# Kernel tuning notes

Hardware: AMD Instinct MI355X
Metric: run time of the kernel (lower is better)

Reference implementation:

```python
import jax, jax.numpy as jnp
import numpy as np

N, CH, K, B = 30000, 96, 81, 8
HIDDEN = max(CH // 4, 8)
EPS = 1e-5


def setup_inputs() -> dict:
    key = jax.random.key(0)
    ks = jax.random.split(key, 12)
    feats = jax.random.normal(ks[0], (N, CH), dtype=jnp.float32)
    nbr_idx = jax.random.randint(ks[1], (N, K), 0, N).astype(jnp.int32)
    batch_ids = jnp.sort(jax.random.randint(ks[2], (N,), 0, B)).astype(jnp.int32)
    s = 1.0 / np.sqrt(CH * 1.0)
    W1 = jax.random.normal(ks[3], (K, CH, CH), dtype=jnp.float32) * s
    W2 = jax.random.normal(ks[4], (K, CH, CH), dtype=jnp.float32) * s
    g1 = jnp.ones((CH,), jnp.float32); b1 = jnp.zeros((CH,), jnp.float32)
    g2 = jnp.ones((CH,), jnp.float32); b2 = jnp.zeros((CH,), jnp.float32)
    fc1_w = jax.random.normal(ks[5], (CH, HIDDEN), dtype=jnp.float32) * s
    fc1_b = jnp.zeros((HIDDEN,), jnp.float32)
    fc2_w = jax.random.normal(ks[6], (HIDDEN, CH), dtype=jnp.float32) * (1.0 / np.sqrt(HIDDEN * 1.0))
    fc2_b = jnp.zeros((CH,), jnp.float32)
    return {"feats": feats, "W1": W1, "g1": g1, "b1": b1, "W2": W2,
            "g2": g2, "b2": b2, "fc1_w": fc1_w, "fc1_b": fc1_b,
            "fc2_w": fc2_w, "fc2_b": fc2_b, "nbr_idx": nbr_idx,
            "batch_ids": batch_ids}


def _sparse_conv(x, W, nbr):
    # gather-matmul-scatter form of MinkowskiConvolution (kernel map shared):
    # g: [N, K, ch] gathered neighbor features; contract each offset's [ch,ch] weight.
    g = x[nbr]
    return jnp.einsum('nkc,kcd->nd', g, W)


def _bn(x, gamma, beta):
    mu = jnp.mean(x, axis=0)
    var = jnp.var(x, axis=0)
    return gamma * (x - mu) * jax.lax.rsqrt(var + EPS) + beta


def _se(x, batch_ids, fc1_w, fc1_b, fc2_w, fc2_b):
    # MinkowskiGlobalAvgPooling: per-sample mean over points
    sums = jax.ops.segment_sum(x, batch_ids, num_segments=B)
    cnts = jax.ops.segment_sum(jnp.ones((x.shape[0], 1), x.dtype), batch_ids, num_segments=B)
    pooled = sums / jnp.maximum(cnts, 1.0)  # [B, ch]
    w = jax.nn.relu(pooled @ fc1_w + fc1_b)
    w = jax.nn.sigmoid(w @ fc2_w + fc2_b)   # [B, ch]
    return x * w[batch_ids]                  # broadcast multiplication


def reference(feats, W1, g1, b1, W2, g2, b2, fc1_w, fc1_b, fc2_w, fc2_b,
              nbr_idx, batch_ids):
    out = jax.nn.relu(_bn(_sparse_conv(feats, W1, nbr_idx), g1, b1))
    out = _bn(_sparse_conv(out, W2, nbr_idx), g2, b2)
    out = _se(out, batch_ids, fc1_w, fc1_b, fc2_w, fc2_b)
    return jax.nn.relu(out + feats)
```

## Files before the change

### kernel.cpp

```cpp
#include <hip/hip_runtime.h>
#include <hip/hip_bf16.h>

#define NPTS 30000
#define CH 96
#define KOFF 81
#define NB 8
#define HID 24
#define EPSV 1e-5f
#define NTILE 469
#define RT 3
#define RSPLIT 157
#define KSPLIT 4

typedef __attribute__((ext_vector_type(8))) short bf16x8;
typedef __attribute__((ext_vector_type(4))) float f32x4;

__device__ __forceinline__ ushort f2bf(float f) {
    union { float f; unsigned int u; } x; x.f = f;
    unsigned int u = x.u;
    unsigned int r = (u + 0x7fffu + ((u >> 16) & 1u)) >> 16;
    return (ushort)r;
}

__device__ __forceinline__ void gll16(const void* g, void* l) {
    __builtin_amdgcn_global_load_lds(
        (const __attribute__((address_space(1))) unsigned int*)g,
        (__attribute__((address_space(3))) unsigned int*)l, 16, 0, 0);
}

__global__ __launch_bounds__(256) void k_prep(const float* __restrict__ feats,
                                              const float* __restrict__ W1,
                                              const float* __restrict__ W2,
                                              const int* __restrict__ nbr,
                                              ushort* __restrict__ featsbf,
                                              float* __restrict__ outbuf,
                                              int* __restrict__ nbrT,
                                              ushort* __restrict__ wt1,
                                              ushort* __restrict__ wt2) {
    __shared__ __align__(16) char smem[36864];
    int bid = blockIdx.x, tid = threadIdx.x;
    if (bid < 2813) {
        int t = bid * 256 + tid;
        if (t < 720000) {
            float4 v = reinterpret_cast<const float4*>(feats)[t];
            ushort4 o;
            o.x = f2bf(v.x); o.y = f2bf(v.y); o.z = f2bf(v.z); o.w = f2bf(v.w);
            reinterpret_cast<ushort4*>(featsbf)[t] = o;
            float4 z = {0.f, 0.f, 0.f, 0.f};
            reinterpret_cast<float4*>(outbuf)[t] = z;
        }
    } else if (bid < 3282) {
        int* lds = (int*)smem;
        int n0 = (bid - 2813) * 64;
        int rows = min(64, NPTS - n0);
        int cnt = rows * 81;
        for (int i = tid; i < cnt; i += 256) lds[i] = nbr[n0 * 81 + i];
        __syncthreads();
        for (int o = tid; o < cnt; o += 256) {
            int kk = o / rows, r = o - kk * rows;
            nbrT[kk * NPTS + n0 + r] = lds[r * 81 + kk];
        }
    } else {
        float* lds = (float*)smem;
        int b = bid - 3282;
        int k = (b < 81) ? b : b - 81;
        const float* src = ((b < 81) ? W1 : W2) + k * 9216;
        ushort* dst = ((b < 81) ? wt1 : wt2) + k * 9216;
        for (int j = tid; j < 9216; j += 256) lds[j] = src[j];
        __syncthreads();
        for (int o = tid; o < 9216; o += 256) {
            int q = o / 768, rem = o - q * 768, d = rem >> 3, j = rem & 7;
            dst[o] = f2bf(lds[(q * 8 + j) * 96 + d]);
        }
    }
}

__global__ __launch_bounds__(256, 2) void k_conv(const ushort* __restrict__ xbf,
                                                 const ushort* __restrict__ wt,
                                                 const int* __restrict__ nbrT,
                                                 float* __restrict__ out) {
    __shared__ __align__(16) ushort Wsm[2][9216];

    const int tid = threadIdx.x;
    const int slice = blockIdx.x / RSPLIT;
    const int rb = blockIdx.x % RSPLIT;
    const int k0 = slice * 20;
    const int k1 = k0 + ((slice == 3) ? 21 : 20);
    const int wave = tid >> 6, lane = tid & 63;
    const int r16 = lane & 15, kg = lane >> 4;
    const int tile0 = rb * RT;

    int nrow[RT];
#pragma unroll
    for (int rt = 0; rt < RT; ++rt) {
        int n = (tile0 + rt) * 64 + wave * 16 + r16;
        nrow[rt] = (n < NPTS) ? n : (NPTS - 1);
    }

    f32x4 zero4 = {0.f, 0.f, 0.f, 0.f};
    f32x4 acc[RT][6];
#pragma unroll
    for (int rt = 0; rt < RT; ++rt)
#pragma unroll
        for (int db = 0; db < 6; ++db) acc[rt][db] = zero4;

    {
        const ushort* wsrc = wt + k0 * 9216 + lane * 8;
#pragma unroll
        for (int t = 0; t < 5; ++t) {
            int i = wave + t * 4;
            if (i < 18) gll16(wsrc + i * 512, Wsm[0] + i * 512);
        }
    }
    int idx[RT];
#pragma unroll
    for (int rt = 0; rt < RT; ++rt) idx[rt] = nbrT[k0 * NPTS + nrow[rt]];
    __syncthreads();

    int cur = 0;
    for (int k = k0; k < k1; ++k) {
        bf16x8 bfrag[18];
#pragma unroll
        for (int c = 0; c < 3; ++c) {
            int q = c * 4 + kg;
#pragma unroll
            for (int db = 0; db < 6; ++db)
                bfrag[c * 6 + db] = *reinterpret_cast<const bf16x8*>(
                    &Wsm[cur][q * 768 + (db * 16 + r16) * 8]);
        }
        bf16x8 afrag[RT][3];
#pragma unroll
        for (int rt = 0; rt < RT; ++rt) {
            const ushort* as = xbf + idx[rt] * 96 + kg * 8;
#pragma unroll
            for (int c = 0; c < 3; ++c)
                afrag[rt][c] = *reinterpret_cast<const bf16x8*>(as + c * 32);
        }
        if (k + 1 < k1) {
            const ushort* wsrc = wt + (k + 1) * 9216 + lane * 8;
#pragma unroll
            for (int t = 0; t < 5; ++t) {
                int i = wave + t * 4;
                if (i < 18) gll16(wsrc + i * 512, Wsm[cur ^ 1] + i * 512);
            }
#pragma unroll
            for (int rt = 0; rt < RT; ++rt) idx[rt] = nbrT[(k + 1) * NPTS + nrow[rt]];
        }
#pragma unroll
        for (int rt = 0; rt < RT; ++rt)
#pragma unroll
            for (int c = 0; c < 3; ++c)
#pragma unroll
                for (int db = 0; db < 6; ++db)
                    acc[rt][db] = __builtin_amdgcn_mfma_f32_16x16x32_bf16(
                        afrag[rt][c], bfrag[c * 6 + db], acc[rt][db], 0, 0, 0);
        __syncthreads();
        cur ^= 1;
    }

#pragma unroll
    for (int rt = 0; rt < RT; ++rt) {
        int rbase = (tile0 + rt) * 64 + wave * 16 + kg * 4;
#pragma unroll
        for (int db = 0; db < 6; ++db) {
            int col = db * 16 + r16;
#pragma unroll
            for (int i = 0; i < 4; ++i) {
                int r = rbase + i;
                if (r < NPTS) atomicAdd(&out[r * 96 + col], acc[rt][db][i]);
            }
        }
    }
}

__device__ __forceinline__ int lowb(const int* __restrict__ bids, int v) {
    int lo = 0, hi = NPTS;
    while (lo < hi) { int m = (lo + hi) >> 1; if (bids[m] < v) lo = m + 1; else hi = m; }
    return lo;
}

template <bool SEG>
__global__ __launch_bounds__(256) void k_stats(const float* __restrict__ y,
                                               const int* __restrict__ bids,
                                               float* __restrict__ ssum,
                                               float* __restrict__ ssq,
                                               float* __restrict__ segsum,
                                               float* __restrict__ cntf) {
    __shared__ float ls[96], lq[96], lg[96];
    int tid = threadIdx.x;
    if (tid < 96) { ls[tid] = 0.f; lq[tid] = 0.f; lg[tid] = 0.f; }
    __syncthreads();

    int b = 0, j, s, e;
    if (SEG) {
        b = blockIdx.x >> 5; j = blockIdx.x & 31;
        s = lowb(bids, b); e = lowb(bids, b + 1);
    } else {
        j = blockIdx.x; s = 0; e = NPTS;
    }
    const int stride = SEG ? (32 * 256) : (256 * 256);
    const int total = (e - s) * 24;
    const int base4 = s * 24;
    const int c40 = j * 256 + tid;

    f32x4 z = {0.f, 0.f, 0.f, 0.f};
    f32x4 sm[3] = {z, z, z}, sq[3] = {z, z, z};
    for (int c4 = c40; c4 < total; c4 += 3 * stride) {
#pragma unroll
        for (int m = 0; m < 3; ++m) {
            int c = c4 + m * stride;
            if (c < total) {
                f32x4 v = reinterpret_cast<const f32x4*>(y)[base4 + c];
                sm[m] += v; sq[m] += v * v;
            }
        }
    }
#pragma unroll
    for (int m = 0; m < 3; ++m) {
        int d0 = ((c40 + m * stride) * 4) % 96;
#pragma unroll
        for (int w = 0; w < 4; ++w) {
            atomicAdd(&ls[d0 + w], sm[m][w]);
            atomicAdd(&lq[d0 + w], sq[m][w]);
            if (SEG) atomicAdd(&lg[d0 + w], sm[m][w]);
        }
    }
    __syncthreads();
    if (tid < 96) {
        atomicAdd(&ssum[tid], ls[tid]);
        atomicAdd(&ssq[tid], lq[tid]);
        if (SEG) atomicAdd(&segsum[b * 96 + tid], lg[tid]);
    }
    if (SEG && tid == 0 && (blockIdx.x & 31) == 0) cntf[b] = (float)(e - s);
}

__global__ void k_bnfinal(const float* __restrict__ ssum, const float* __restrict__ ssq,
                          const float* __restrict__ g, const float* __restrict__ b,
                          float* __restrict__ scale, float* __restrict__ shift) {
    int t = threadIdx.x;
    if (t >= 96) return;
    float mean = ssum[t] * (1.0f / NPTS);
    float var = ssq[t] * (1.0f / NPTS) - mean * mean;
    float sc = g[t] * rsqrtf(var + EPSV);
    scale[t] = sc;
    shift[t] = b[t] - mean * sc;
}

__global__ void k_apply1(float* __restrict__ x, const float* __restrict__ scale,
                         const float* __restrict__ shift, ushort* __restrict__ h) {
    int t = blockIdx.x * 256 + threadIdx.x;
    if (t >= 720000) return;
    float4 v = reinterpret_cast<const float4*>(x)[t];
    int d0 = (t * 4) % 96;
    ushort4 o;
    o.x = f2bf(fmaxf(v.x * scale[d0] + shift[d0], 0.f));
    o.y = f2bf(fmaxf(v.y * scale[d0 + 1] + shift[d0 + 1], 0.f));
    o.z = f2bf(fmaxf(v.z * scale[d0 + 2] + shift[d0 + 2], 0.f));
    o.w = f2bf(fmaxf(v.w * scale[d0 + 3] + shift[d0 + 3], 0.f));
    reinterpret_cast<ushort4*>(h)[t] = o;
    float4 z = {0.f, 0.f, 0.f, 0.f};
    reinterpret_cast<float4*>(x)[t] = z;
}

__global__ void k_se(const float* __restrict__ segsum, const float* __restrict__ cnt,
                     const float* __restrict__ scale, const float* __restrict__ shift,
                     const float* __restrict__ fc1w, const float* __restrict__ fc1b,
                     const float* __restrict__ fc2w, const float* __restrict__ fc2b,
                     float* __restrict__ sew) {
    __shared__ float pooled[NB][96];
    __shared__ float hid[NB][HID];
    int t = threadIdx.x;
    for (int i = t; i < NB * 96; i += 256) {
        int b = i / 96, d = i - b * 96;
        pooled[b][d] = segsum[i] / fmaxf(cnt[b], 1.f) * scale[d] + shift[d];
    }
    __syncthreads();
    if (t < NB * HID) {
        int b = t / HID, h = t - b * HID;
        float s = fc1b[h];
        for (int d = 0; d < 96; ++d) s += pooled[b][d] * fc1w[d * HID + h];
        hid[b][h] = fmaxf(s, 0.f);
    }
    __syncthreads();
    for (int i = t; i < NB * 96; i += 256) {
        int b = i / 96, d = i - b * 96;
        float s = fc2b[d];
        for (int h = 0; h < HID; ++h) s += hid[b][h] * fc2w[h * 96 + d];
        sew[i] = 1.f / (1.f + expf(-s));
    }
}

__global__ void k_final(const float* __restrict__ out2, const float* __restrict__ feats,
                        const float* __restrict__ scale, const float* __restrict__ shift,
                        const float* __restrict__ sew, const int* __restrict__ bids,
                        float* __restrict__ out) {
    int t = blockIdx.x * 256 + threadIdx.x;
    if (t >= 720000) return;
    int e0 = t * 4;
    int n = e0 / 96;
    int d0 = e0 - n * 96;
    int b = bids[n];
    const float* w = sew + b * 96;
    float4 v = reinterpret_cast<const float4*>(out2)[t];
    float4 f = reinterpret_cast<const float4*>(feats)[t];
    float4 o;
    o.x = fmaxf((v.x * scale[d0] + shift[d0]) * w[d0] + f.x, 0.f);
    o.y = fmaxf((v.y * scale[d0 + 1] + shift[d0 + 1]) * w[d0 + 1] + f.y, 0.f);
    o.z = fmaxf((v.z * scale[d0 + 2] + shift[d0 + 2]) * w[d0 + 2] + f.z, 0.f);
    o.w = fmaxf((v.w * scale[d0 + 3] + shift[d0 + 3]) * w[d0 + 3] + f.w, 0.f);
    reinterpret_cast<float4*>(out)[t] = o;
}


extern "C" void kernel_launch(void* const* d_in, const int* in_sizes, int n_in,
                              void* d_out, int out_size, void* d_ws, size_t ws_size,
                              hipStream_t stream) {
    const float* feats = (const float*)d_in[0];
    const float* W1 = (const float*)d_in[1];
    const float* g1 = (const float*)d_in[2];
    const float* b1 = (const float*)d_in[3];
    const float* W2 = (const float*)d_in[4];
    const float* g2 = (const float*)d_in[5];
    const float* b2 = (const float*)d_in[6];
    const float* fc1w = (const float*)d_in[7];
    const float* fc1b = (const float*)d_in[8];
    const float* fc2w = (const float*)d_in[9];
    const float* fc2b = (const float*)d_in[10];
    const int* nbr = (const int*)d_in[11];
    const int* bids = (const int*)d_in[12];
    float* out = (float*)d_out;

    char* ws = (char*)d_ws;
    ushort* featsbf = (ushort*)(ws + 0);
    ushort* wt1 = (ushort*)(ws + 5760000);
    ushort* wt2 = (ushort*)(ws + 7252992);
    int* nbrT = (int*)(ws + 8745984);
    float* outbuf = (float*)(ws + 18465984);
    ushort* h1bf = (ushort*)(ws + 29985984);
    float* small = (float*)(ws + 35745984);
    float* sum1 = small + 0;
    float* sq1 = small + 96;
    float* sum2 = small + 192;
    float* sq2 = small + 288;
    float* scale1 = small + 384;
    float* shift1 = small + 480;
    float* scale2 = small + 576;
    float* shift2 = small + 672;
    float* segsum = small + 768;
    float* cntf = small + 1536;
    float* sew = small + 1544;

    const int gE = 2813;
    const int gC = KSPLIT * RSPLIT;

    hipMemsetAsync(small, 0, 16384, stream);
    k_prep<<<3444, 256, 0, stream>>>(feats, W1, W2, nbr, featsbf, outbuf, nbrT, wt1, wt2);

    k_conv<<<gC, 256, 0, stream>>>(featsbf, wt1, nbrT, outbuf);
    k_stats<false><<<256, 256, 0, stream>>>(outbuf, bids, sum1, sq1, segsum, cntf);
    k_bnfinal<<<1, 128, 0, stream>>>(sum1, sq1, g1, b1, scale1, shift1);
    k_apply1<<<gE, 256, 0, stream>>>(outbuf, scale1, shift1, h1bf);

    k_conv<<<gC, 256, 0, stream>>>(h1bf, wt2, nbrT, outbuf);
    k_stats<true><<<256, 256, 0, stream>>>(outbuf, bids, sum2, sq2, segsum, cntf);
    k_bnfinal<<<1, 128, 0, stream>>>(sum2, sq2, g2, b2, scale2, shift2);

    k_se<<<1, 256, 0, stream>>>(segsum, cntf, scale2, shift2, fc1w, fc1b, fc2w, fc2b, sew);
    k_final<<<gE, 256, 0, stream>>>(outbuf, feats, scale2, shift2, sew, bids, out);
}
```

Measured before the change: 370.8 us.

## Split conv over 8 kernel-offset slices and fold BN finalize into consumers

The conv grid doubles its split over kernel offsets (8 slices of about 10 offsets) and launch bounds now request 4 blocks per SM, to raise occupancy and parallelism. The gather loads of neighbour features are issued before the LDS weight-fragment reads, so global latency overlaps with the LDS reads. The separate single-block BN-finalize kernels are removed. Each block of k_apply1, k_se and k_final now recomputes scale and shift into shared memory, saving two launches at the cost of redundant per-block work and an extra barrier. Doubling the K-split doubles atomic or partial-sum traffic into the output buffer, and the higher occupancy target may force register spills given the large per-thread accumulator and fragment arrays.

Measured after the change: 1.266 ms. 241% more time.

```diff
diff --git a/kernel.cpp b/kernel.cpp
--- a/kernel.cpp
+++ b/kernel.cpp
@@ -10,7 +10,7 @@
 #define NTILE 469
 #define RT 3
 #define RSPLIT 157
-#define KSPLIT 4
+#define KSPLIT 8
 
 typedef __attribute__((ext_vector_type(8))) short bf16x8;
 typedef __attribute__((ext_vector_type(4))) float f32x4;
@@ -26,6 +26,22 @@
     __builtin_amdgcn_global_load_lds(
         (const __attribute__((address_space(1))) unsigned int*)g,
         (__attribute__((address_space(3))) unsigned int*)l, 16, 0, 0);
+}
+
+__device__ __forceinline__ void bn_coeffs(const float* __restrict__ ssum,
+                                          const float* __restrict__ ssq,
+                                          const float* __restrict__ g,
+                                          const float* __restrict__ b,
+                                          float* s_scale, float* s_shift) {
+    int t = threadIdx.x;
+    if (t < 96) {
+        float mean = ssum[t] * (1.0f / NPTS);
+        float var = ssq[t] * (1.0f / NPTS) - mean * mean;
+        float sc = g[t] * rsqrtf(var + EPSV);
+        s_scale[t] = sc;
+        s_shift[t] = b[t] - mean * sc;
+    }
+    __syncthreads();
 }
 
 __global__ __launch_bounds__(256) void k_prep(const float* __restrict__ feats,
@@ -75,7 +91,7 @@
     }
 }
 
-__global__ __launch_bounds__(256, 2) void k_conv(const ushort* __restrict__ xbf,
+__global__ __launch_bounds__(256, 4) void k_conv(const ushort* __restrict__ xbf,
                                                  const ushort* __restrict__ wt,
                                                  const int* __restrict__ nbrT,
                                                  float* __restrict__ out) {
@@ -84,8 +100,8 @@
     const int tid = threadIdx.x;
     const int slice = blockIdx.x / RSPLIT;
     const int rb = blockIdx.x % RSPLIT;
-    const int k0 = slice * 20;
-    const int k1 = k0 + ((slice == 3) ? 21 : 20);
+    const int k0 = slice * 10;
+    const int k1 = k0 + ((slice == 7) ? 11 : 10);
     const int wave = tid >> 6, lane = tid & 63;
     const int r16 = lane & 15, kg = lane >> 4;
     const int tile0 = rb * RT;
@@ -119,6 +135,14 @@
 
     int cur = 0;
     for (int k = k0; k < k1; ++k) {
+        bf16x8 afrag[RT][3];
+#pragma unroll
+        for (int rt = 0; rt < RT; ++rt) {
+            const ushort* as = xbf + idx[rt] * 96 + kg * 8;
+#pragma unroll
+            for (int c = 0; c < 3; ++c)
+                afrag[rt][c] = *reinterpret_cast<const bf16x8*>(as + c * 32);
+        }
         bf16x8 bfrag[18];
 #pragma unroll
         for (int c = 0; c < 3; ++c) {
@@ -127,14 +151,6 @@
             for (int db = 0; db < 6; ++db)
                 bfrag[c * 6 + db] = *reinterpret_cast<const bf16x8*>(
                     &Wsm[cur][q * 768 + (db * 16 + r16) * 8]);
-        }
-        bf16x8 afrag[RT][3];
-#pragma unroll
-        for (int rt = 0; rt < RT; ++rt) {
-            const ushort* as = xbf + idx[rt] * 96 + kg * 8;
-#pragma unroll
-            for (int c = 0; c < 3; ++c)
-                afrag[rt][c] = *reinterpret_cast<const bf16x8*>(as + c * 32);
         }
         if (k + 1 < k1) {
             const ushort* wsrc = wt + (k + 1) * 9216 + lane * 8;
@@ -234,20 +250,12 @@
     if (SEG && tid == 0 && (blockIdx.x & 31) == 0) cntf[b] = (float)(e - s);
 }
 
-__global__ void k_bnfinal(const float* __restrict__ ssum, const float* __restrict__ ssq,
-                          const float* __restrict__ g, const float* __restrict__ b,
-                          float* __restrict__ scale, float* __restrict__ shift) {
-    int t = threadIdx.x;
-    if (t >= 96) return;
-    float mean = ssum[t] * (1.0f / NPTS);
-    float var = ssq[t] * (1.0f / NPTS) - mean * mean;
-    float sc = g[t] * rsqrtf(var + EPSV);
-    scale[t] = sc;
-    shift[t] = b[t] - mean * sc;
-}
-
-__global__ void k_apply1(float* __restrict__ x, const float* __restrict__ scale,
-                         const float* __restrict__ shift, ushort* __restrict__ h) {
+__global__ void k_apply1(float* __restrict__ x,
+                         const float* __restrict__ ssum, const float* __restrict__ ssq,
+                         const float* __restrict__ g, const float* __restrict__ b,
+                         ushort* __restrict__ h) {
+    __shared__ float scale[96], shift[96];
+    bn_coeffs(ssum, ssq, g, b, scale, shift);
     int t = blockIdx.x * 256 + threadIdx.x;
     if (t >= 720000) return;
     float4 v = reinterpret_cast<const float4*>(x)[t];
@@ -263,44 +271,50 @@
 }
 
 __global__ void k_se(const float* __restrict__ segsum, const float* __restrict__ cnt,
-                     const float* __restrict__ scale, const float* __restrict__ shift,
+                     const float* __restrict__ ssum, const float* __restrict__ ssq,
+                     const float* __restrict__ g, const float* __restrict__ b,
                      const float* __restrict__ fc1w, const float* __restrict__ fc1b,
                      const float* __restrict__ fc2w, const float* __restrict__ fc2b,
                      float* __restrict__ sew) {
+    __shared__ float scale[96], shift[96];
     __shared__ float pooled[NB][96];
     __shared__ float hid[NB][HID];
+    bn_coeffs(ssum, ssq, g, b, scale, shift);
     int t = threadIdx.x;
     for (int i = t; i < NB * 96; i += 256) {
-        int b = i / 96, d = i - b * 96;
-        pooled[b][d] = segsum[i] / fmaxf(cnt[b], 1.f) * scale[d] + shift[d];
+        int bb = i / 96, d = i - bb * 96;
+        pooled[bb][d] = segsum[i] / fmaxf(cnt[bb], 1.f) * scale[d] + shift[d];
     }
     __syncthreads();
     if (t < NB * HID) {
-        int b = t / HID, h = t - b * HID;
+        int bb = t / HID, h = t - bb * HID;
         float s = fc1b[h];
-        for (int d = 0; d < 96; ++d) s += pooled[b][d] * fc1w[d * HID + h];
-        hid[b][h] = fmaxf(s, 0.f);
+        for (int d = 0; d < 96; ++d) s += pooled[bb][d] * fc1w[d * HID + h];
+        hid[bb][h] = fmaxf(s, 0.f);
     }
     __syncthreads();
     for (int i = t; i < NB * 96; i += 256) {
-        int b = i / 96, d = i - b * 96;
+        int bb = i / 96, d = i - bb * 96;
         float s = fc2b[d];
-        for (int h = 0; h < HID; ++h) s += hid[b][h] * fc2w[h * 96 + d];
+        for (int h = 0; h < HID; ++h) s += hid[bb][h] * fc2w[h * 96 + d];
         sew[i] = 1.f / (1.f + expf(-s));
     }
 }
 
 __global__ void k_final(const float* __restrict__ out2, const float* __restrict__ feats,
-                        const float* __restrict__ scale, const float* __restrict__ shift,
+                        const float* __restrict__ ssum, const float* __restrict__ ssq,
+                        const float* __restrict__ g, const float* __restrict__ b,
                         const float* __restrict__ sew, const int* __restrict__ bids,
                         float* __restrict__ out) {
+    __shared__ float scale[96], shift[96];
+    bn_coeffs(ssum, ssq, g, b, scale, shift);
     int t = blockIdx.x * 256 + threadIdx.x;
     if (t >= 720000) return;
     int e0 = t * 4;
     int n = e0 / 96;
     int d0 = e0 - n * 96;
-    int b = bids[n];
-    const float* w = sew + b * 96;
+    int bb = bids[n];
+    const float* w = sew + bb * 96;
     float4 v = reinterpret_cast<const float4*>(out2)[t];
     float4 f = reinterpret_cast<const float4*>(feats)[t];
     float4 o;
@@ -342,10 +356,6 @@
     float* sq1 = small + 96;
     float* sum2 = small + 192;
     float* sq2 = small + 288;
-    float* scale1 = small + 384;
-    float* shift1 = small + 480;
-    float* scale2 = small + 576;
-    float* shift2 = small + 672;
     float* segsum = small + 768;
     float* cntf = small + 1536;
     float* sew = small + 1544;
@@ -358,13 +368,11 @@
 
     k_conv<<<gC, 256, 0, stream>>>(featsbf, wt1, nbrT, outbuf);
     k_stats<false><<<256, 256, 0, stream>>>(outbuf, bids, sum1, sq1, segsum, cntf);
-    k_bnfinal<<<1, 128, 0, stream>>>(sum1, sq1, g1, b1, scale1, shift1);
-    k_apply1<<<gE, 256, 0, stream>>>(outbuf, scale1, shift1, h1bf);
+    k_apply1<<<gE, 256, 0, stream>>>(outbuf, sum1, sq1, g1, b1, h1bf);
 
     k_conv<<<gC, 256, 0, stream>>>(h1bf, wt2, nbrT, outbuf);
     k_stats<true><<<256, 256, 0, stream>>>(outbuf, bids, sum2, sq2, segsum, cntf);
-    k_bnfinal<<<1, 128, 0, stream>>>(sum2, sq2, g2, b2, scale2, shift2);
-
-    k_se<<<1, 256, 0, stream>>>(segsum, cntf, scale2, shift2, fc1w, fc1b, fc2w, fc2b, sew);
-    k_final<<<gE, 256, 0, stream>>>(outbuf, feats, scale2, shift2, sew, bids, out);
-}
+
+    k_se<<<1, 256, 0, stream>>>(segsum, cntf, sum2, sq2, g2, b2, fc1w, fc1b, fc2w, fc2b, sew);
+    k_final<<<gE, 256, 0, stream>>>(outbuf, feats, sum2, sq2, g2, b2, sew, bids, out);
+}
```
